# Performance work log

Hardware: AMD Instinct MI355X
Metric: run time of the kernel (lower is better)

The kernel has to match this reference:

```python
import jax, jax.numpy as jnp
import numpy as np

B, L, C = 8, 2048, 256
D = C // 8  # qk head dim = 32


def _attn(q, k, v, scale):
    # q:[B,L,D] k:[B,L,D] v:[B,L,Dv] -> [B,L,Dv]
    scores = jnp.einsum('bld,bmd->blm', q, k) / scale
    w = jax.nn.softmax(scores, axis=-1)
    return jnp.einsum('blm,bmd->bld', w, v)


def setup_inputs() -> dict:
    key = jax.random.key(0)
    ks = jax.random.split(key, 16)
    he = lambda k, cin, cout: jax.random.normal(k, (cin, cout), jnp.float32) * np.sqrt(2.0 / cin)
    inp = {'x': jax.random.normal(ks[0], (B, L, C, 2), jnp.float32)}
    # 12 1x1 conv kernels (no bias): Q/K -> C//8, V -> C, for 4 attention blocks
    dims = [D, D, C, D, D, C, D, D, C, D, D, C]
    for i, dout in enumerate(dims):
        inp[f'w{i+1}'] = he(ks[i + 1], C, dout)
    inp['alpha'] = jnp.zeros((1,), jnp.float32)
    inp['gamma'] = jnp.zeros((1,), jnp.float32)
    return inp


def reference(x, w1, w2, w3, w4, w5, w6, w7, w8, w9, w10, w11, w12, alpha, gamma):
    ecg = x[:, :, :, 0]  # [B,L,C]
    pcg = x[:, :, :, 1]
    proj = lambda f, w: jnp.einsum('blc,cd->bld', f, w)  # 1x1 conv, no bias
    scale = jnp.sqrt(jnp.asarray(D, x.dtype))

    # ECG intra-attention
    qkv_ecg_intra = _attn(proj(ecg, w1), proj(ecg, w2), proj(ecg, w3), scale)
    # ECG inter-attention (Q from ECG, K/V from PCG)
    qkv_ecg_inter = _attn(proj(ecg, w4), proj(pcg, w5), proj(pcg, w6), scale)
    ecg_out = qkv_ecg_inter + alpha * qkv_ecg_intra

    # PCG intra-attention
    qkv_pcg_intra = _attn(proj(pcg, w7), proj(pcg, w8), proj(pcg, w9), scale)
    # PCG inter-attention (Q from PCG, K/V from ECG)
    qkv_pcg_inter = _attn(proj(pcg, w10), proj(ecg, w11), proj(ecg, w12), scale)
    pcg_out = qkv_pcg_inter + gamma * qkv_pcg_intra

    return jnp.concatenate([ecg_out, pcg_out], axis=-1)  # [B,L,2C]
```

## Files before the change

kernel.cpp:

```cpp
#include <hip/hip_runtime.h>


typedef __bf16 v8bf __attribute__((ext_vector_type(8)));
typedef float  v16f __attribute__((ext_vector_type(16)));
typedef unsigned int u32;

typedef __attribute__((address_space(1))) const void gvoid;
typedef __attribute__((address_space(3))) void svoid;

#define QSCALE 0.25500526817276613f

union frag_u { u32 d[4]; v8bf v; };
union pk_u { unsigned short s[2]; u32 d; };

static __device__ inline u32 pack_bf16(float x, float y) {
  pk_u u;
  __bf16 a = (__bf16)x, b = (__bf16)y;
  u.s[0] = *(unsigned short*)&a;
  u.s[1] = *(unsigned short*)&b;
  return u.d;
}

__global__ __launch_bounds__(256) void deint_kernel(const float* __restrict__ x,
                                                    __bf16* __restrict__ xe,
                                                    __bf16* __restrict__ xp) {
  const size_t i = (size_t)blockIdx.x * 256 + threadIdx.x;
  const float4* xin = (const float4*)(x + i * 16);
  float4 a = xin[0], b = xin[1], c = xin[2], d = xin[3];
  v8bf ev, pv;
  ev[0]=(__bf16)a.x; ev[1]=(__bf16)a.z; ev[2]=(__bf16)b.x; ev[3]=(__bf16)b.z;
  ev[4]=(__bf16)c.x; ev[5]=(__bf16)c.z; ev[6]=(__bf16)d.x; ev[7]=(__bf16)d.z;
  pv[0]=(__bf16)a.y; pv[1]=(__bf16)a.w; pv[2]=(__bf16)b.y; pv[3]=(__bf16)b.w;
  pv[4]=(__bf16)c.y; pv[5]=(__bf16)c.w; pv[6]=(__bf16)d.y; pv[7]=(__bf16)d.w;
  *(v8bf*)(xe + i * 8) = ev;
  *(v8bf*)(xp + i * 8) = pv;
}

struct ProjArgs {
  const __bf16* xe;
  const __bf16* xp;
  const float* w[12];
  __bf16* q[4];
  __bf16* k[4];
  __bf16* vt[4];
  const float* alpha;
  const float* gamma;
};

__global__ __launch_bounds__(256) void proj_kernel(ProjArgs pa) {
  const int job = blockIdx.x;
  const int rb  = blockIdx.y * 128;
  const int tid = threadIdx.x;
  const int lane = tid & 63, w = tid >> 6;
  const int l31 = lane & 31, lh = lane >> 5;
  const int l7 = lane & 7, l8 = lane >> 3;

  if (job >= 4) {
    const int vi = (job - 4) >> 2;
    if (vi == 0 && pa.alpha[0] == 0.0f) return;
    if (vi == 3 && pa.gamma[0] == 0.0f) return;
  }

  __shared__ __bf16 lds_b[64][264];
  __shared__ __bf16 lds_a[2][128 * 64];

  int src, dout, wc0[2], vcol0 = 0, vmode = 0;
  const float* wp[2];
  __bf16* dqk[2] = {nullptr, nullptr};
  __bf16* vdst = nullptr;
  float sc = 1.0f;
  if (job < 4) {
    dout = 32; wc0[0] = 0; wc0[1] = 0;
    switch (job) {
      case 0: src=0; wp[0]=pa.w[0]; wp[1]=pa.w[3];  dqk[0]=pa.q[0]; dqk[1]=pa.q[1]; sc=QSCALE; break;
      case 1: src=0; wp[0]=pa.w[1]; wp[1]=pa.w[10]; dqk[0]=pa.k[0]; dqk[1]=pa.k[3]; break;
      case 2: src=1; wp[0]=pa.w[6]; wp[1]=pa.w[9];  dqk[0]=pa.q[2]; dqk[1]=pa.q[3]; sc=QSCALE; break;
      default:src=1; wp[0]=pa.w[4]; wp[1]=pa.w[7];  dqk[0]=pa.k[1]; dqk[1]=pa.k[2]; break;
    }
  } else {
    const int vi = (job - 4) >> 2, t = (job - 4) & 3;
    const int widx = (vi==0) ? 2 : (vi==1) ? 11 : (vi==2) ? 5 : 8;
    const int vbuf = (vi==0) ? 0 : (vi==1) ? 3  : (vi==2) ? 1 : 2;
    dout = 256; vmode = 1; src = vi >> 1;
    wp[0] = pa.w[widx]; wp[1] = pa.w[widx];
    wc0[0] = t*64; wc0[1] = t*64 + 32;
    vcol0 = t*64; vdst = pa.vt[vbuf];
  }

  for (int h = 0; h < 2; ++h) {
    const float* wgt = wp[h]; const int c0 = wc0[h];
    for (int i = tid; i < 32*256; i += 256) {
      int n = i & 31, kk = i >> 5;
      lds_b[h*32 + n][kk] = (__bf16)wgt[(size_t)kk*dout + c0 + n];
    }
  }

  const __bf16* X = src ? pa.xp : pa.xe;
  const char* agbase = (const char*)(X + (size_t)rb*256) + (size_t)(l7 ^ l8)*16
                     + (size_t)l8*512;

#define STAGE_A(buf, kb)                                                        \
  {                                                                             \
    const char* g = agbase + (size_t)(kb)*128;                                  \
    _Pragma("unroll")                                                           \
    for (int i = 0; i < 4; ++i)                                                 \
      __builtin_amdgcn_global_load_lds(                                         \
          (gvoid*)(g + (size_t)(w*4 + i)*8*512),                                \
          (svoid*)&lds_a[buf][((w*4 + i)*8)*64 + lane*8], 16, 0, 0);            \
  }

  STAGE_A(0, 0)
  __syncthreads();

  v16f acc[2];
#pragma unroll
  for (int n = 0; n < 2; ++n)
#pragma unroll
    for (int i = 0; i < 16; ++i) acc[n][i] = 0.f;

  for (int kb = 0; kb < 4; ++kb) {
    if (kb < 3) STAGE_A((kb + 1) & 1, kb + 1)
    const __bf16* ab = &lds_a[kb & 1][0];
#pragma unroll
    for (int kk = 0; kk < 4; ++kk) {
      const v8bf af = *(const v8bf*)&ab[(w*32 + l31)*64 + (((kk*2 + lh) ^ (l31 & 7))*8)];
#pragma unroll
      for (int nt = 0; nt < 2; ++nt) {
        const v8bf bf = *(const v8bf*)&lds_b[nt*32 + l31][kb*64 + kk*16 + lh*8];
        acc[nt] = __builtin_amdgcn_mfma_f32_32x32x16_bf16(af, bf, acc[nt], 0, 0, 0);
      }
    }
    __syncthreads();
  }

  if (!vmode) {
#pragma unroll
    for (int nt = 0; nt < 2; ++nt) {
      __bf16* dst = dqk[nt];
#pragma unroll
      for (int r = 0; r < 16; ++r) {
        const int row = rb + w*32 + (r & 3) + 8*(r >> 2) + 4*lh;
        dst[(size_t)row*32 + l31] = (__bf16)(acc[nt][r] * sc);
      }
    }
  } else {
    __bf16 (*lds_t)[136] = (__bf16 (*)[136])&lds_a[0][0];
#pragma unroll
    for (int nt = 0; nt < 2; ++nt) {
#pragma unroll
      for (int r = 0; r < 16; ++r) {
        const int row = w*32 + (r & 3) + 8*(r >> 2) + 4*lh;
        lds_t[nt*32 + l31][row] = (__bf16)acc[nt][r];
      }
    }
    __syncthreads();
    const int bb = rb >> 11, ll0 = rb & 2047;
    const int nt0 = vcol0 >> 5;
    const size_t tbase = (size_t)(bb*32 + (ll0 >> 6));
    for (int i = tid; i < 1024; i += 256) {
      const int ktl = i >> 9, s = i & 511;
      const int h = s >> 8, kc2 = (s >> 5) & 7, v5 = s & 31;
      const int vrow = h*32 + v5, krow = ktl*64 + kc2*8;
      *(int4*)&vdst[((tbase + ktl)*2048 + (size_t)((nt0 + h)*8 + kc2)*32 + v5) * 8] =
          *(const int4*)&lds_t[vrow][krow];
    }
  }
}

struct FlashArgs {
  const __bf16* q[4];
  const __bf16* k[4];
  const __bf16* v[4];
  const float* alpha;
  const float* gamma;
  float* out;
};

__global__ __launch_bounds__(256, 4) void flash_half(FlashArgs fa) {
  const int flat = blockIdx.x;
  const int pair = flat & 31, qt = flat >> 5;
  const int att = pair & 3, bb = pair >> 2;
  const int tid = threadIdx.x;
  const int lane = tid & 63, w = tid >> 6;
  const int qsub = w >> 1, kh = w & 1;
  const int l31 = lane & 31, lh = lane >> 5;

  const float av = fa.alpha[0], gv = fa.gamma[0];
  int att_e, nt0;
  if (att == 0)      { if (av != 0.0f) return; att_e = 1; nt0 = 4; }
  else if (att == 1) { if (av != 0.0f) return; att_e = 1; nt0 = 0; }
  else if (att == 2) { if (gv != 0.0f) return; att_e = 3; nt0 = 4; }
  else               { if (gv != 0.0f) return; att_e = 3; nt0 = 0; }

  __shared__ __bf16 v_lds[2][8192];
  __shared__ float dlds[2][32];

  const __bf16* Qp = fa.q[att_e] + (size_t)(bb*2048 + qt*64 + qsub*32 + l31)*32;
  const __bf16* Kb = fa.k[att_e] + (size_t)bb*2048*32;
  const char* vgbase = (const char*)(fa.v[att_e] + (size_t)bb*32*16384)
                     + (size_t)(nt0*256 + w*256 + lane)*16;
  float* outp = fa.out + (size_t)(bb*2048 + qt*64 + qsub*32)*512
              + (att_e >> 1)*256 + nt0*32;

  const v8bf qf0 = *(const v8bf*)&Qp[lh*8];
  const v8bf qf1 = *(const v8bf*)&Qp[16 + lh*8];

#define HSTAGE(buf_, kt_)                                                       \
  {                                                                             \
    const char* g = vgbase + (size_t)(kt_)*32768;                               \
    _Pragma("unroll")                                                           \
    for (int i = 0; i < 4; ++i)                                                 \
      __builtin_amdgcn_global_load_lds(                                         \
          (gvoid*)(g + (size_t)i*1024),                                         \
          (svoid*)&v_lds[buf_][(w*256 + 64*i)*8 + lane*8], 16, 0, 0);           \
  }

#define HLOADK(a_, b_, kt_)                                                     \
  {                                                                             \
    const size_t kr = (size_t)((kt_)*64 + kh*32 + l31) * 32;                    \
    a_ = *(const v8bf*)&Kb[kr + lh*8];                                          \
    b_ = *(const v8bf*)&Kb[kr + 16 + lh*8];                                     \
  }

  v16f acc[4];
#pragma unroll
  for (int n = 0; n < 4; ++n)
#pragma unroll
    for (int i = 0; i < 16; ++i) acc[n][i] = 0.f;
  float den_s = 0.f;

  v8bf kfc0, kfc1;
  HLOADK(kfc0, kfc1, 0)
  HSTAGE(0, 0)
  __syncthreads();

#pragma unroll 1
  for (int kt = 0; kt < 32; ++kt) {
    const int cur = kt & 1;
    v8bf kfn0, kfn1;
    if (kt < 31) {
      HLOADK(kfn0, kfn1, kt + 1)
      HSTAGE(cur ^ 1, kt + 1)
    }

    v16f st;
#pragma unroll
    for (int i = 0; i < 16; ++i) st[i] = 0.f;
    st = __builtin_amdgcn_mfma_f32_32x32x16_bf16(kfc0, qf0, st, 0, 0, 0);
    st = __builtin_amdgcn_mfma_f32_32x32x16_bf16(kfc1, qf1, st, 0, 0, 0);

    u32 pk[8];
#pragma unroll
    for (int i = 0; i < 8; ++i) {
      const float e0 = __builtin_exp2f(st[2*i]);
      const float e1 = __builtin_exp2f(st[2*i + 1]);
      den_s += e0 + e1;
      pk[i] = pack_bf16(e0, e1);
    }

    v8bf pf[2];
#pragma unroll
    for (int f2 = 0; f2 < 2; ++f2) {
      u32 a0 = pk[f2*4 + 0], b0 = pk[f2*4 + 2];
      u32 a1 = pk[f2*4 + 1], b1 = pk[f2*4 + 3];
      asm("v_permlane32_swap_b32 %0, %1" : "+v"(a0), "+v"(b0));
      asm("v_permlane32_swap_b32 %0, %1" : "+v"(a1), "+v"(b1));
      frag_u fu;
      fu.d[0] = a0; fu.d[1] = a1; fu.d[2] = b0; fu.d[3] = b1;
      pf[f2] = fu.v;
    }

    const __bf16* vb = &v_lds[cur][0];
#pragma unroll
    for (int j = 0; j < 2; ++j) {
      const int kc = kh*2 + j;
#pragma unroll
      for (int nt = 0; nt < 4; ++nt) {
        const v8bf vf = *(const v8bf*)&vb[(nt*256 + kc*64 + lane)*8];
        acc[nt] = __builtin_amdgcn_mfma_f32_32x32x16_bf16(pf[j], vf, acc[nt], 0, 0, 0);
      }
    }

    __syncthreads();
    if (kt < 31) { kfc0 = kfn0; kfc1 = kfn1; }
  }

  const float den_half = den_s + __shfl_xor(den_s, 32, 64);
  float* alds = (float*)&v_lds[0][0];
  if (kh) {
    if (lane < 32) dlds[qsub][l31] = den_half;
#pragma unroll
    for (int nt = 0; nt < 4; ++nt)
#pragma unroll
      for (int r = 0; r < 16; ++r)
        alds[qsub*4096 + nt*1024 + r*64 + lane] = acc[nt][r];
  }
  __syncthreads();
  if (!kh) {
    const float den_full = den_half + dlds[qsub][l31];
#pragma unroll
    for (int r = 0; r < 16; ++r) {
      const int row = (r & 3) + 8*(r >> 2) + 4*lh;
      const float f = 1.0f / __shfl(den_full, row, 64);
#pragma unroll
      for (int nt = 0; nt < 4; ++nt)
        outp[(size_t)row*512 + nt*32 + l31] =
            (acc[nt][r] + alds[qsub*4096 + nt*1024 + r*64 + lane]) * f;
    }
  }

#undef HSTAGE
#undef HLOADK
}

template<int NTN>
__device__ __forceinline__ void flash_body(
    const __bf16* __restrict__ Qp, const __bf16* __restrict__ Kb,
    const char* __restrict__ vgbase, float scv, float* __restrict__ outp,
    __bf16* __restrict__ lds0, int lane, int w, int l31, int lh) {

  __bf16* vb0 = lds0;
  __bf16* vb1 = lds0 + NTN*2048;

  const v8bf qf0 = *(const v8bf*)&Qp[lh*8];
  const v8bf qf1 = *(const v8bf*)&Qp[16 + lh*8];

#define STAGE_V(dst_, kt_)                                                      \
  {                                                                             \
    const char* g = vgbase + (size_t)(kt_)*32768;                               \
    _Pragma("unroll")                                                           \
    for (int i = 0; i < NTN; ++i)                                               \
      __builtin_amdgcn_global_load_lds(                                         \
          (gvoid*)(g + (size_t)i*1024),                                         \
          (svoid*)&dst_[(w*NTN*64 + 64*i)*8 + lane*8], 16, 0, 0);               \
  }

  v16f acc[NTN];
#pragma unroll
  for (int n = 0; n < NTN; ++n)
#pragma unroll
    for (int i = 0; i < 16; ++i) acc[n][i] = 0.f;

  float den_s = 0.f;
  v8bf pf[4];
  v8bf kf00, kf01, kf10, kf11;
  v16f st0, st1;
  u32 pk0[8], pk1[8];

#define LOADK(kt_)                                                              \
  {                                                                             \
    const int kb_ = (kt_) * 64;                                                 \
    kf00 = *(const v8bf*)&Kb[((size_t)(kb_ +      l31))*32 +      lh*8];        \
    kf01 = *(const v8bf*)&Kb[((size_t)(kb_ +      l31))*32 + 16 + lh*8];        \
    kf10 = *(const v8bf*)&Kb[((size_t)(kb_ + 32 + l31))*32 +      lh*8];        \
    kf11 = *(const v8bf*)&Kb[((size_t)(kb_ + 32 + l31))*32 + 16 + lh*8];        \
  }

#define SMFMA                                                                   \
  {                                                                             \
    _Pragma("unroll")                                                           \
    for (int i = 0; i < 16; ++i) { st0[i] = 0.f; st1[i] = 0.f; }                \
    st0 = __builtin_amdgcn_mfma_f32_32x32x16_bf16(kf00, qf0, st0, 0, 0, 0);     \
    st0 = __builtin_amdgcn_mfma_f32_32x32x16_bf16(kf01, qf1, st0, 0, 0, 0);     \
    st1 = __builtin_amdgcn_mfma_f32_32x32x16_bf16(kf10, qf0, st1, 0, 0, 0);     \
    st1 = __builtin_amdgcn_mfma_f32_32x32x16_bf16(kf11, qf1, st1, 0, 0, 0);     \
  }

#define EXPH(st_, pk_)                                                          \
  _Pragma("unroll")                                                             \
  for (int i = 0; i < 8; ++i) {                                                 \
    const float e0 = __builtin_exp2f(st_[2*i]);                                 \
    const float e1 = __builtin_exp2f(st_[2*i + 1]);                             \
    den_s += e0 + e1;                                                           \
    pk_[i] = pack_bf16(e0, e1);                                                 \
  }

#define XCHG(pk_, o_)                                                           \
  _Pragma("unroll")                                                             \
  for (int f2 = 0; f2 < 2; ++f2) {                                              \
    u32 a0 = pk_[f2*4 + 0], b0 = pk_[f2*4 + 2];                                 \
    u32 a1 = pk_[f2*4 + 1], b1 = pk_[f2*4 + 3];                                 \
    asm("v_permlane32_swap_b32 %0, %1" : "+v"(a0), "+v"(b0));                   \
    asm("v_permlane32_swap_b32 %0, %1" : "+v"(a1), "+v"(b1));                   \
    frag_u fu;                                                                  \
    fu.d[0] = a0; fu.d[1] = a1; fu.d[2] = b0; fu.d[3] = b1;                     \
    pf[(o_) + f2] = fu.v;                                                       \
  }

#define PVBLK(kc_, vb_)                                                         \
  _Pragma("unroll")                                                             \
  for (int nt = 0; nt < NTN; ++nt) {                                            \
    const v8bf vf = *(const v8bf*)&vb_[(nt*256 + (kc_)*64 + lane)*8];           \
    acc[nt] = __builtin_amdgcn_mfma_f32_32x32x16_bf16(pf[kc_], vf, acc[nt], 0, 0, 0); \
  }

  LOADK(0)
  STAGE_V(vb0, 0)
  SMFMA
  EXPH(st0, pk0)
  EXPH(st1, pk1)
  XCHG(pk0, 0)
  XCHG(pk1, 2)
  __syncthreads();

  for (int kt = 0; kt < 31; ++kt) {
    const int cur = kt & 1;
    LOADK(kt + 1)
    if (cur) { STAGE_V(vb0, kt + 1) } else { STAGE_V(vb1, kt + 1) }
    const __bf16* vb = cur ? vb1 : vb0;

    PVBLK(0, vb)
    SMFMA
    PVBLK(1, vb)
    EXPH(st0, pk0)
    PVBLK(2, vb)
    EXPH(st1, pk1)
    XCHG(pk0, 0)
    PVBLK(3, vb)
    XCHG(pk1, 2)

    __syncthreads();
  }

  {
    PVBLK(0, vb1)
    PVBLK(1, vb1)
    PVBLK(2, vb1)
    PVBLK(3, vb1)
  }

  const float den_full = den_s + __shfl_xor(den_s, 32, 64);
#pragma unroll
  for (int r = 0; r < 16; ++r) {
    const int row = (r & 3) + 8*(r >> 2) + 4*lh;
    const float f = scv / __shfl(den_full, row, 64);
#pragma unroll
    for (int nt = 0; nt < NTN; ++nt)
      unsafeAtomicAdd(&outp[(size_t)row*512 + nt*32 + l31], acc[nt][r] * f);
  }

#undef STAGE_V
#undef LOADK
#undef SMFMA
#undef EXPH
#undef XCHG
#undef PVBLK
}

__global__ __launch_bounds__(256, 2) void flash_full(FlashArgs fa) {
  const int flat = blockIdx.x;
  const int pair = flat & 31, qt = flat >> 5;
  const int att = pair & 3, bb = pair >> 2;
  const int tid = threadIdx.x;
  const int lane = tid & 63, w = tid >> 6;
  const int l31 = lane & 31, lh = lane >> 5;

  const float av = fa.alpha[0], gv = fa.gamma[0];
  float scv = 1.0f;
  if (att == 0)      { if (av == 0.0f) return; scv = av; }
  else if (att == 1) { if (av == 0.0f) return; }
  else if (att == 2) { if (gv == 0.0f) return; scv = gv; }
  else               { if (gv == 0.0f) return; }

  __shared__ __bf16 v_lds[2][16384];

  const __bf16* Qp = fa.q[att] + (size_t)(bb*2048 + qt*128 + w*32 + l31)*32;
  const __bf16* Kb = fa.k[att] + (size_t)bb*2048*32;
  const char* vgbase = (const char*)(fa.v[att] + (size_t)bb*32*16384)
                     + (size_t)(w*512 + lane)*16;
  float* outp = fa.out + (size_t)(bb*2048 + qt*128 + w*32)*512 + (att >> 1)*256;

  flash_body<8>(Qp, Kb, vgbase, scv, outp, &v_lds[0][0], lane, w, l31, lh);
}

extern "C" void kernel_launch(void* const* d_in, const int* in_sizes, int n_in,
                              void* d_out, int out_size, void* d_ws, size_t ws_size,
                              hipStream_t stream) {
  (void)in_sizes; (void)n_in; (void)out_size; (void)ws_size;

  __bf16* wsp = (__bf16*)d_ws;
  const size_t XE = (size_t)16384 * 256;
  const size_t QK = (size_t)16384 * 32;
  const size_t VT = (size_t)8 * 32 * 16384;

  __bf16* xe = wsp;
  __bf16* xp = wsp + XE;

  ProjArgs pa;
  pa.xe = xe; pa.xp = xp;
  const float* x = (const float*)d_in[0];
  for (int i = 0; i < 12; ++i) pa.w[i] = (const float*)d_in[1 + i];
  __bf16* base = wsp + 2*XE;
  for (int i = 0; i < 4; ++i) pa.q[i]  = base + (size_t)i * QK;
  for (int i = 0; i < 4; ++i) pa.k[i]  = base + (size_t)(4 + i) * QK;
  for (int i = 0; i < 4; ++i) pa.vt[i] = base + 8*QK + (size_t)i * VT;
  pa.alpha = (const float*)d_in[13];
  pa.gamma = (const float*)d_in[14];

  hipMemsetAsync(d_out, 0, (size_t)8*2048*512*4, stream);
  hipLaunchKernelGGL(deint_kernel, dim3(2048), dim3(256), 0, stream, x, xe, xp);
  hipLaunchKernelGGL(proj_kernel, dim3(20, 128), dim3(256), 0, stream, pa);

  FlashArgs fl;
  for (int i = 0; i < 4; ++i) { fl.q[i] = pa.q[i]; fl.k[i] = pa.k[i]; fl.v[i] = pa.vt[i]; }
  fl.alpha = (const float*)d_in[13];
  fl.gamma = (const float*)d_in[14];
  fl.out = (float*)d_out;
  hipLaunchKernelGGL(flash_half, dim3(1024), dim3(256), 0, stream, fl);
  hipLaunchKernelGGL(flash_full, dim3(512), dim3(256), 0, stream, fl);
}
```

Before: 223.3 us.

## Split flash_half over V column halves, fuse full-path pairs, drop output memset

The zero-alpha/gamma path kernel now splits each block's V output columns into two halves. This doubles the grid to 2048 blocks, halves LDS and accumulator use, and raises the occupancy hint to 5. The general flash_full path now runs both the inter and intra attention for a pair in one block, with plain stores followed by an accumulating read-modify-write instead of atomics. That change removes the need for the output memset. The cost is that Q and K work is repeated across the two column halves, and the softmax exp work is recomputed twice per query tile.

```diff
diff --git a/kernel.cpp b/kernel.cpp
--- a/kernel.cpp
+++ b/kernel.cpp
@@ -176,9 +176,11 @@
   float* out;
 };
 
-__global__ __launch_bounds__(256, 4) void flash_half(FlashArgs fa) {
+__global__ __launch_bounds__(256, 5) void flash_half(FlashArgs fa) {
   const int flat = blockIdx.x;
-  const int pair = flat & 31, qt = flat >> 5;
+  const int pair = flat & 31;
+  const int vh = (flat >> 5) & 1;
+  const int qt = flat >> 6;
   const int att = pair & 3, bb = pair >> 2;
   const int tid = threadIdx.x;
   const int lane = tid & 63, w = tid >> 6;
@@ -191,16 +193,17 @@
   else if (att == 1) { if (av != 0.0f) return; att_e = 1; nt0 = 0; }
   else if (att == 2) { if (gv != 0.0f) return; att_e = 3; nt0 = 4; }
   else               { if (gv != 0.0f) return; att_e = 3; nt0 = 0; }
-
-  __shared__ __bf16 v_lds[2][8192];
+  const int nt0f = nt0 + vh*2;
+
+  __shared__ __bf16 v_lds[2][4096];
   __shared__ float dlds[2][32];
 
   const __bf16* Qp = fa.q[att_e] + (size_t)(bb*2048 + qt*64 + qsub*32 + l31)*32;
   const __bf16* Kb = fa.k[att_e] + (size_t)bb*2048*32;
   const char* vgbase = (const char*)(fa.v[att_e] + (size_t)bb*32*16384)
-                     + (size_t)(nt0*256 + w*256 + lane)*16;
+                     + (size_t)(nt0f*256 + w*128 + lane)*16;
   float* outp = fa.out + (size_t)(bb*2048 + qt*64 + qsub*32)*512
-              + (att_e >> 1)*256 + nt0*32;
+              + (att_e >> 1)*256 + nt0f*32;
 
   const v8bf qf0 = *(const v8bf*)&Qp[lh*8];
   const v8bf qf1 = *(const v8bf*)&Qp[16 + lh*8];
@@ -209,10 +212,10 @@
   {                                                                             \
     const char* g = vgbase + (size_t)(kt_)*32768;                               \
     _Pragma("unroll")                                                           \
-    for (int i = 0; i < 4; ++i)                                                 \
+    for (int i = 0; i < 2; ++i)                                                 \
       __builtin_amdgcn_global_load_lds(                                         \
           (gvoid*)(g + (size_t)i*1024),                                         \
-          (svoid*)&v_lds[buf_][(w*256 + 64*i)*8 + lane*8], 16, 0, 0);           \
+          (svoid*)&v_lds[buf_][(w*128 + 64*i)*8 + lane*8], 16, 0, 0);           \
   }
 
 #define HLOADK(a_, b_, kt_)                                                     \
@@ -222,9 +225,9 @@
     b_ = *(const v8bf*)&Kb[kr + 16 + lh*8];                                     \
   }
 
-  v16f acc[4];
-#pragma unroll
-  for (int n = 0; n < 4; ++n)
+  v16f acc[2];
+#pragma unroll
+  for (int n = 0; n < 2; ++n)
 #pragma unroll
     for (int i = 0; i < 16; ++i) acc[n][i] = 0.f;
   float den_s = 0.f;
@@ -275,7 +278,7 @@
     for (int j = 0; j < 2; ++j) {
       const int kc = kh*2 + j;
 #pragma unroll
-      for (int nt = 0; nt < 4; ++nt) {
+      for (int nt = 0; nt < 2; ++nt) {
         const v8bf vf = *(const v8bf*)&vb[(nt*256 + kc*64 + lane)*8];
         acc[nt] = __builtin_amdgcn_mfma_f32_32x32x16_bf16(pf[j], vf, acc[nt], 0, 0, 0);
       }
@@ -290,10 +293,10 @@
   if (kh) {
     if (lane < 32) dlds[qsub][l31] = den_half;
 #pragma unroll
-    for (int nt = 0; nt < 4; ++nt)
+    for (int nt = 0; nt < 2; ++nt)
 #pragma unroll
       for (int r = 0; r < 16; ++r)
-        alds[qsub*4096 + nt*1024 + r*64 + lane] = acc[nt][r];
+        alds[qsub*2048 + nt*1024 + r*64 + lane] = acc[nt][r];
   }
   __syncthreads();
   if (!kh) {
@@ -303,9 +306,9 @@
       const int row = (r & 3) + 8*(r >> 2) + 4*lh;
       const float f = 1.0f / __shfl(den_full, row, 64);
 #pragma unroll
-      for (int nt = 0; nt < 4; ++nt)
+      for (int nt = 0; nt < 2; ++nt)
         outp[(size_t)row*512 + nt*32 + l31] =
-            (acc[nt][r] + alds[qsub*4096 + nt*1024 + r*64 + lane]) * f;
+            (acc[nt][r] + alds[qsub*2048 + nt*1024 + r*64 + lane]) * f;
     }
   }
 
@@ -313,7 +316,7 @@
 #undef HLOADK
 }
 
-template<int NTN>
+template<int NTN, bool ACCUM>
 __device__ __forceinline__ void flash_body(
     const __bf16* __restrict__ Qp, const __bf16* __restrict__ Kb,
     const char* __restrict__ vgbase, float scv, float* __restrict__ outp,
@@ -435,8 +438,11 @@
     const int row = (r & 3) + 8*(r >> 2) + 4*lh;
     const float f = scv / __shfl(den_full, row, 64);
 #pragma unroll
-    for (int nt = 0; nt < NTN; ++nt)
-      unsafeAtomicAdd(&outp[(size_t)row*512 + nt*32 + l31], acc[nt][r] * f);
+    for (int nt = 0; nt < NTN; ++nt) {
+      const size_t idx = (size_t)row*512 + nt*32 + l31;
+      const float v = acc[nt][r] * f;
+      outp[idx] = ACCUM ? (outp[idx] + v) : v;
+    }
   }
 
 #undef STAGE_V
@@ -451,26 +457,35 @@
   const int flat = blockIdx.x;
   const int pair = flat & 31, qt = flat >> 5;
   const int att = pair & 3, bb = pair >> 2;
+  if (!(att & 1)) return;
+
+  const float scv = (att == 1) ? fa.alpha[0] : fa.gamma[0];
+  if (scv == 0.0f) return;
+
   const int tid = threadIdx.x;
   const int lane = tid & 63, w = tid >> 6;
   const int l31 = lane & 31, lh = lane >> 5;
 
-  const float av = fa.alpha[0], gv = fa.gamma[0];
-  float scv = 1.0f;
-  if (att == 0)      { if (av == 0.0f) return; scv = av; }
-  else if (att == 1) { if (av == 0.0f) return; }
-  else if (att == 2) { if (gv == 0.0f) return; scv = gv; }
-  else               { if (gv == 0.0f) return; }
-
   __shared__ __bf16 v_lds[2][16384];
 
-  const __bf16* Qp = fa.q[att] + (size_t)(bb*2048 + qt*128 + w*32 + l31)*32;
-  const __bf16* Kb = fa.k[att] + (size_t)bb*2048*32;
-  const char* vgbase = (const char*)(fa.v[att] + (size_t)bb*32*16384)
-                     + (size_t)(w*512 + lane)*16;
   float* outp = fa.out + (size_t)(bb*2048 + qt*128 + w*32)*512 + (att >> 1)*256;
 
-  flash_body<8>(Qp, Kb, vgbase, scv, outp, &v_lds[0][0], lane, w, l31, lh);
+  {
+    const __bf16* Qp = fa.q[att] + (size_t)(bb*2048 + qt*128 + w*32 + l31)*32;
+    const __bf16* Kb = fa.k[att] + (size_t)bb*2048*32;
+    const char* vgbase = (const char*)(fa.v[att] + (size_t)bb*32*16384)
+                       + (size_t)(w*512 + lane)*16;
+    flash_body<8, false>(Qp, Kb, vgbase, 1.0f, outp, &v_lds[0][0], lane, w, l31, lh);
+  }
+  __syncthreads();
+  {
+    const int ai = att - 1;
+    const __bf16* Qp = fa.q[ai] + (size_t)(bb*2048 + qt*128 + w*32 + l31)*32;
+    const __bf16* Kb = fa.k[ai] + (size_t)bb*2048*32;
+    const char* vgbase = (const char*)(fa.v[ai] + (size_t)bb*32*16384)
+                       + (size_t)(w*512 + lane)*16;
+    flash_body<8, true>(Qp, Kb, vgbase, scv, outp, &v_lds[0][0], lane, w, l31, lh);
+  }
 }
 
 extern "C" void kernel_launch(void* const* d_in, const int* in_sizes, int n_in,
@@ -497,7 +512,6 @@
   pa.alpha = (const float*)d_in[13];
   pa.gamma = (const float*)d_in[14];
 
-  hipMemsetAsync(d_out, 0, (size_t)8*2048*512*4, stream);
   hipLaunchKernelGGL(deint_kernel, dim3(2048), dim3(256), 0, stream, x, xe, xp);
   hipLaunchKernelGGL(proj_kernel, dim3(20, 128), dim3(256), 0, stream, pa);
 
@@ -506,6 +520,6 @@
   fl.alpha = (const float*)d_in[13];
   fl.gamma = (const float*)d_in[14];
   fl.out = (float*)d_out;
-  hipLaunchKernelGGL(flash_half, dim3(1024), dim3(256), 0, stream, fl);
+  hipLaunchKernelGGL(flash_half, dim3(2048), dim3(256), 0, stream, fl);
   hipLaunchKernelGGL(flash_full, dim3(512), dim3(256), 0, stream, fl);
 }
```

Result: slower. 244.0 us (+9.2%).
